# Kernel optimization log

Measured on AMD Instinct MI355X. Metric: run time of the kernel, lower is better.

The kernel has to match this reference:

```python
import jax, jax.numpy as jnp
import numpy as np

B, T, N = 2, 512, 512
H = 64          # hidden_dim
S = 8           # static_dim
C = 8           # coord_dim
DYN = 4         # dynamic feature dim (hard-coded in module)
SELF_LOOP_W = 1.0


def setup_inputs() -> dict:
    key = jax.random.key(0)
    ks = jax.random.split(key, 12)
    x = jax.random.normal(ks[0], (B, T, N), dtype=jnp.float32)
    mask = jax.random.randint(ks[1], (B, T, N), 0, 2).astype(jnp.float32)
    static_context = jax.random.normal(ks[2], (N, S), dtype=jnp.float32)
    node_coords = jax.random.normal(ks[3], (N, C), dtype=jnp.float32)
    sc = 0.1
    W1 = jax.random.normal(ks[4], (DYN + S, H), dtype=jnp.float32) * sc
    b1 = jnp.zeros((H,), dtype=jnp.float32)
    W2 = jax.random.normal(ks[5], (H, H), dtype=jnp.float32) * sc
    b2 = jnp.zeros((H,), dtype=jnp.float32)
    W3 = jax.random.normal(ks[6], (4 * H, H), dtype=jnp.float32) * sc
    b3 = jnp.zeros((H,), dtype=jnp.float32)
    W4 = jax.random.normal(ks[7], (H, 1), dtype=jnp.float32) * sc
    b4 = jnp.zeros((1,), dtype=jnp.float32)
    return {"x": x, "mask": mask, "static_context": static_context,
            "node_coords": node_coords, "W1": W1, "b1": b1, "W2": W2,
            "b2": b2, "W3": W3, "b3": b3, "W4": W4, "b4": b4}


def _dynamic_context(x, mask):
    observed = 1.0 - mask                                  # (B,T,N)
    count = jnp.maximum(observed.sum(axis=1), 1.0)          # (B,N)
    mean = (x * observed).sum(axis=1) / count               # (B,N)
    centered = (x - mean[:, None, :]) * observed
    std = jnp.sqrt((centered ** 2).sum(axis=1) / count + 1e-6)
    # last observed value per node
    t_idx = jnp.arange(x.shape[1], dtype=x.dtype)[None, :, None]
    latest = jnp.argmax(t_idx * observed, axis=1)           # (B,N) int
    last = jnp.take_along_axis(x, latest[:, None, :], axis=1)[:, 0, :]
    missing_ratio = mask.mean(axis=1)                       # (B,N)
    return jnp.stack([mean, std, last, missing_ratio], axis=-1)  # (B,N,4)


def _prior_adjacency(node_coords):
    diff = node_coords[:, None, :] - node_coords[None, :, :]  # (N,N,C)
    d2 = (diff ** 2).sum(-1)
    dist = jnp.where(d2 > 0, jnp.sqrt(jnp.where(d2 > 0, d2, 1.0)), 0.0)
    prior = 1.0 / (1.0 + dist)
    eye = jnp.eye(node_coords.shape[0], dtype=node_coords.dtype)
    return prior * (1.0 - eye)


def reference(x, mask, static_context, node_coords, W1, b1, W2, b2, W3, b3, W4, b4):
    batch = x.shape[0]
    node_dynamic = _dynamic_context(x, mask)                         # (B,N,4)
    node_static = jnp.broadcast_to(static_context[None], (batch,) + static_context.shape)
    feats = jnp.concatenate([node_dynamic, node_static], axis=-1)    # (B,N,4+S)
    h = jax.nn.relu(feats @ W1 + b1)
    node_repr = jax.nn.relu(h @ W2 + b2)                              # (B,N,H)

    h_i = node_repr[:, :, None, :]                                    # (B,N,1,H)
    h_j = node_repr[:, None, :, :]                                    # (B,1,N,H)
    hi = jnp.broadcast_to(h_i, (batch, N, N, H))
    hj = jnp.broadcast_to(h_j, (batch, N, N, H))
    pair = jnp.concatenate([hi, hj, jnp.abs(hi - hj), hi * hj], axis=-1)  # (B,N,N,4H)
    e = jax.nn.relu(pair @ W3 + b3)
    edge_mod = jax.nn.relu((e @ W4 + b4)[..., 0])                     # (B,N,N)

    prior = _prior_adjacency(node_coords)[None]                       # (1,N,N)
    eye = jnp.eye(N, dtype=x.dtype)[None]
    adapt = edge_mod * prior + eye * SELF_LOOP_W
    degree = jnp.maximum(adapt.sum(axis=-1), 1e-6)                    # (B,N)
    inv_sqrt = degree ** -0.5
    return inv_sqrt[:, :, None] * adapt * inv_sqrt[:, None, :]
```

## Files before the change

### kernel.cpp

```cpp
#include <hip/hip_runtime.h>
#include <hip/hip_bf16.h>
#include <math.h>

#define B_ 2
#define T_ 512
#define N_ 512
#define H_ 64

typedef __attribute__((ext_vector_type(8))) short short8;
typedef __attribute__((ext_vector_type(4))) float floatx4;

__device__ inline short f2bf(float f) {
    union { float f; unsigned u; } v; v.f = f;
    unsigned r = (v.u + 0x7fffu + ((v.u >> 16) & 1u)) >> 16;
    return (short)r;
}

__global__ void prep_kernel(const float* __restrict__ x, const float* __restrict__ mask,
                            const float* __restrict__ coords, const float* __restrict__ W3,
                            float* __restrict__ part, float* __restrict__ prior,
                            short* __restrict__ W3p) {
    int blk = blockIdx.x;
    if (blk < 512) {
        int b  = blk >> 8;
        int nc = (blk >> 5) & 7;
        int tc = blk & 31;
        int tn = threadIdx.x & 63;
        int tt = threadIdx.x >> 6;
        int n  = nc * 64 + tn;

        float sx = 0.f, sxx = 0.f, cnt = 0.f, msum = 0.f, bv = 0.f, bt = -1.f;
#pragma unroll
        for (int it = 0; it < 4; it++) {
            int t = tc * 16 + it * 4 + tt;
            int off = (b * T_ + t) * N_ + n;
            float xv = x[off];
            float mv = mask[off];
            float obs = 1.f - mv;
            sx   += xv * obs;
            sxx  += xv * xv * obs;
            cnt  += obs;
            msum += mv;
            if (obs > 0.5f) { bt = (float)t; bv = xv; }
        }

        __shared__ float red[6][4][64];
        red[0][tt][tn] = sx;  red[1][tt][tn] = sxx; red[2][tt][tn] = cnt;
        red[3][tt][tn] = msum; red[4][tt][tn] = bv; red[5][tt][tn] = bt;
        __syncthreads();

        if (threadIdx.x < 64) {
            float Sx = 0.f, Sxx = 0.f, Cnt = 0.f, Ms = 0.f, Bv = 0.f, Bt = -1.f;
#pragma unroll
            for (int u = 0; u < 4; u++) {
                Sx  += red[0][u][tn];
                Sxx += red[1][u][tn];
                Cnt += red[2][u][tn];
                Ms  += red[3][u][tn];
                float btu = red[5][u][tn];
                if (btu > Bt) { Bt = btu; Bv = red[4][u][tn]; }
            }
            const int plane = B_ * 32 * N_;
            int base = (b * 32 + tc) * N_ + n;
            part[0 * plane + base] = Sx;
            part[1 * plane + base] = Sxx;
            part[2 * plane + base] = Cnt;
            part[3 * plane + base] = Ms;
            part[4 * plane + base] = Bv;
            part[5 * plane + base] = Bt;
        }
    } else if (blk < 1536) {
        int idx = (blk - 512) * 256 + threadIdx.x;
        int i = idx >> 9, j = idx & (N_ - 1);
        float d2 = 0.f;
#pragma unroll
        for (int c = 0; c < 8; c++) {
            float df = coords[i * 8 + c] - coords[j * 8 + c];
            d2 += df * df;
        }
        float dist = (d2 > 0.f) ? sqrtf(d2) : 0.f;
        prior[idx] = (i == j) ? 0.f : 1.f / (1.f + dist);
    } else {
        int k = (blk - 1536) * 256 + threadIdx.x;
        int t = k & 7;
        int l = (k >> 3) & 63;
        int f = k >> 9;
        int s = f >> 2, nt = f & 3;
        int quad = l >> 4, col = l & 15;
        W3p[k] = f2bf(W3[(128 + s * 32 + quad * 8 + t) * H_ + nt * 16 + col]);
    }
}

__global__ __launch_bounds__(64) void node_kernel(
        const float* __restrict__ part, const float* __restrict__ x,
        const float* __restrict__ sc,
        const float* __restrict__ W1, const float* __restrict__ b1,
        const float* __restrict__ W2, const float* __restrict__ b2,
        const float* __restrict__ W3,
        float* __restrict__ nr, float* __restrict__ P, float* __restrict__ Qp) {
    int blk = blockIdx.x;
    int b = blk >> 9;
    int n = blk & (N_ - 1);
    int o = threadIdx.x;

    __shared__ float f[12];
    __shared__ float h[H_];
    __shared__ float r[H_];

    {
        const int plane = B_ * 32 * N_;
        float Sx = 0.f, Sxx = 0.f, Cnt = 0.f, Ms = 0.f, Bv = 0.f, Bt = -1.f;
        if (o < 32) {
            int base = (b * 32 + o) * N_ + n;
            Sx  = part[0 * plane + base];
            Sxx = part[1 * plane + base];
            Cnt = part[2 * plane + base];
            Ms  = part[3 * plane + base];
            Bv  = part[4 * plane + base];
            Bt  = part[5 * plane + base];
        }
#pragma unroll
        for (int off = 1; off < 32; off <<= 1) {
            Sx  += __shfl_xor(Sx, off);
            Sxx += __shfl_xor(Sxx, off);
            Cnt += __shfl_xor(Cnt, off);
            Ms  += __shfl_xor(Ms, off);
            float obt = __shfl_xor(Bt, off);
            float obv = __shfl_xor(Bv, off);
            if (obt > Bt) { Bt = obt; Bv = obv; }
        }
        if (o == 0) {
            float count = fmaxf(Cnt, 1.f);
            float mean  = Sx / count;
            float var   = (Sxx - 2.f * mean * Sx + mean * mean * Cnt) / count;
            float stdv  = sqrtf(fmaxf(var, 0.f) + 1e-6f);
            float last  = (Bt >= 0.f) ? Bv : x[b * T_ * N_ + n];
            f[0] = mean; f[1] = stdv; f[2] = last; f[3] = Ms * (1.f / (float)T_);
        }
        if (o >= 4 && o < 12) f[o] = sc[n * 8 + (o - 4)];
    }
    __syncthreads();

    float a = b1[o];
#pragma unroll
    for (int k = 0; k < 12; k++) a += f[k] * W1[k * H_ + o];
    h[o] = fmaxf(a, 0.f);
    __syncthreads();

    float a2 = b2[o];
#pragma unroll 8
    for (int k = 0; k < H_; k++) a2 += h[k] * W2[k * H_ + o];
    float rv = fmaxf(a2, 0.f);
    r[o] = rv;
    nr[(b * N_ + n) * H_ + o] = rv;
    __syncthreads();

    float p = 0.f, q = 0.f;
#pragma unroll 8
    for (int k = 0; k < H_; k++) {
        float rk = r[k];
        p += rk * W3[k * H_ + o];
        q += rk * W3[(H_ + k) * H_ + o];
    }
    P[(b * N_ + n) * H_ + o] = p;
    Qp[(b * N_ + n) * H_ + (o & 15) * 4 + (o >> 4)] = q;
}

__global__ __launch_bounds__(256) void pair_mfma_kernel(
        const float* __restrict__ nr, const float* __restrict__ P,
        const float* __restrict__ Qp, const short* __restrict__ W3p,
        const float* __restrict__ b3, const float* __restrict__ W4,
        const float* __restrict__ b4, const float* __restrict__ prior,
        float* __restrict__ adapt, float* __restrict__ degree) {
    int blk = blockIdx.x;
    int b = blk >> 9;
    int i = blk & (N_ - 1);
    int tid = threadIdx.x;
    int w = tid >> 6;
    int l = tid & 63;
    int col = l & 15;
    int quad = l >> 4;

    short8 bf[4][4];
#pragma unroll
    for (int s = 0; s < 4; s++)
#pragma unroll
        for (int nt = 0; nt < 4; nt++)
            bf[s][nt] = *(const short8*)(W3p + (((s * 4 + nt) * 64 + l) << 3));

    const float* hi_row = nr + (b * N_ + i) * H_;
    floatx4 hiA0 = *(const floatx4*)(hi_row + quad * 8);
    floatx4 hiA1 = *(const floatx4*)(hi_row + quad * 8 + 4);
    floatx4 hiB0 = *(const floatx4*)(hi_row + 32 + quad * 8);
    floatx4 hiB1 = *(const floatx4*)(hi_row + 32 + quad * 8 + 4);

    float pb3[4], w4v[4];
#pragma unroll
    for (int nt = 0; nt < 4; nt++) {
        int o = nt * 16 + col;
        pb3[nt] = P[(b * N_ + i) * H_ + o] + b3[o];
        w4v[nt] = W4[o];
    }
    float b4s = b4[0];
    const float* prow = prior + i * N_;
    const float* nrb = nr + (b * N_) * H_;
    float rsum = 0.f;

    floatx4 hA0, hA1, hB0, hB1;
    {
        const float* p0 = nrb + (w * 128 + col) * H_;
        hA0 = *(const floatx4*)(p0 + quad * 8);
        hA1 = *(const floatx4*)(p0 + quad * 8 + 4);
        hB0 = *(const floatx4*)(p0 + 32 + quad * 8);
        hB1 = *(const floatx4*)(p0 + 32 + quad * 8 + 4);
    }

#pragma unroll
    for (int mt = 0; mt < 8; mt++) {
        int j0 = w * 128 + mt * 16;

        floatx4 nA0, nA1, nB0, nB1;
        if (mt < 7) {
            const float* pn = nrb + (j0 + 16 + col) * H_;
            nA0 = *(const floatx4*)(pn + quad * 8);
            nA1 = *(const floatx4*)(pn + quad * 8 + 4);
            nB0 = *(const floatx4*)(pn + 32 + quad * 8);
            nB1 = *(const floatx4*)(pn + 32 + quad * 8 + 4);
        }

        floatx4 pv = *(const floatx4*)(prow + j0 + quad * 4);
        floatx4 qv[4];
#pragma unroll
        for (int r = 0; r < 4; r++)
            qv[r] = *(const floatx4*)(Qp + (b * N_ + j0 + quad * 4 + r) * H_ + col * 4);

        union { short8 s; __hip_bfloat162 h[4]; } a0, a1, a2, a3;
#pragma unroll
        for (int t = 0; t < 2; t++) {
            a0.h[t]     = __float22bfloat162_rn(make_float2(fabsf(hiA0[2*t] - hA0[2*t]),
                                                            fabsf(hiA0[2*t+1] - hA0[2*t+1])));
            a0.h[t + 2] = __float22bfloat162_rn(make_float2(fabsf(hiA1[2*t] - hA1[2*t]),
                                                            fabsf(hiA1[2*t+1] - hA1[2*t+1])));
            a1.h[t]     = __float22bfloat162_rn(make_float2(fabsf(hiB0[2*t] - hB0[2*t]),
                                                            fabsf(hiB0[2*t+1] - hB0[2*t+1])));
            a1.h[t + 2] = __float22bfloat162_rn(make_float2(fabsf(hiB1[2*t] - hB1[2*t]),
                                                            fabsf(hiB1[2*t+1] - hB1[2*t+1])));
            a2.h[t]     = __float22bfloat162_rn(make_float2(hiA0[2*t] * hA0[2*t],
                                                            hiA0[2*t+1] * hA0[2*t+1]));
            a2.h[t + 2] = __float22bfloat162_rn(make_float2(hiA1[2*t] * hA1[2*t],
                                                            hiA1[2*t+1] * hA1[2*t+1]));
            a3.h[t]     = __float22bfloat162_rn(make_float2(hiB0[2*t] * hB0[2*t],
                                                            hiB0[2*t+1] * hB0[2*t+1]));
            a3.h[t + 2] = __float22bfloat162_rn(make_float2(hiB1[2*t] * hB1[2*t],
                                                            hiB1[2*t+1] * hB1[2*t+1]));
        }

        floatx4 acc[4];
#pragma unroll
        for (int nt = 0; nt < 4; nt++) acc[nt] = (floatx4){0.f, 0.f, 0.f, 0.f};
#pragma unroll
        for (int nt = 0; nt < 4; nt++) {
            acc[nt] = __builtin_amdgcn_mfma_f32_16x16x32_bf16(a0.s, bf[0][nt], acc[nt], 0, 0, 0);
            acc[nt] = __builtin_amdgcn_mfma_f32_16x16x32_bf16(a1.s, bf[1][nt], acc[nt], 0, 0, 0);
            acc[nt] = __builtin_amdgcn_mfma_f32_16x16x32_bf16(a2.s, bf[2][nt], acc[nt], 0, 0, 0);
            acc[nt] = __builtin_amdgcn_mfma_f32_16x16x32_bf16(a3.s, bf[3][nt], acc[nt], 0, 0, 0);
        }

        float ed[4];
#pragma unroll
        for (int r = 0; r < 4; r++) {
            int j = j0 + quad * 4 + r;
            float p = 0.f;
#pragma unroll
            for (int nt = 0; nt < 4; nt++)
                p += fmaxf(acc[nt][r] + pb3[nt] + qv[r][nt], 0.f) * w4v[nt];
            p += __shfl_xor(p, 1);
            p += __shfl_xor(p, 2);
            p += __shfl_xor(p, 4);
            p += __shfl_xor(p, 8);
            float edge = fmaxf(p + b4s, 0.f);
            float ad = (j == i) ? 1.0f : edge * pv[r];
            ed[r] = ad;
            rsum += ad;
        }
        if (col == 0) {
            *(floatx4*)&adapt[(size_t)(b * N_ + i) * N_ + j0 + quad * 4] =
                (floatx4){ed[0], ed[1], ed[2], ed[3]};
        }

        if (mt < 7) { hA0 = nA0; hA1 = nA1; hB0 = nB0; hB1 = nB1; }
    }

    rsum += __shfl_xor(rsum, 16);
    rsum += __shfl_xor(rsum, 32);
    __shared__ float sRow[4];
    if (l == 0) sRow[w] = rsum;
    __syncthreads();
    if (tid == 0) degree[b * N_ + i] = sRow[0] + sRow[1] + sRow[2] + sRow[3];
}

__global__ void norm_kernel(const float* __restrict__ adapt, const float* __restrict__ deg,
                            float* __restrict__ out) {
    int idx = blockIdx.x * 256 + threadIdx.x;
    int b = idx >> 16;
    int r = (idx >> 7) & (N_ - 1);
    int c4 = (idx & 127) << 2;
    float dr = rsqrtf(fmaxf(deg[b * N_ + r], 1e-6f));
    floatx4 a = *(const floatx4*)(adapt + ((size_t)idx << 2));
    floatx4 o;
#pragma unroll
    for (int k = 0; k < 4; k++)
        o[k] = dr * a[k] * rsqrtf(fmaxf(deg[b * N_ + c4 + k], 1e-6f));
    *(floatx4*)(out + ((size_t)idx << 2)) = o;
}

extern "C" void kernel_launch(void* const* d_in, const int* in_sizes, int n_in,
                              void* d_out, int out_size, void* d_ws, size_t ws_size,
                              hipStream_t stream) {
    const float* x      = (const float*)d_in[0];
    const float* mask   = (const float*)d_in[1];
    const float* sc     = (const float*)d_in[2];
    const float* coords = (const float*)d_in[3];
    const float* W1 = (const float*)d_in[4];
    const float* b1 = (const float*)d_in[5];
    const float* W2 = (const float*)d_in[6];
    const float* b2 = (const float*)d_in[7];
    const float* W3 = (const float*)d_in[8];
    const float* b3 = (const float*)d_in[9];
    const float* W4 = (const float*)d_in[10];
    const float* b4 = (const float*)d_in[11];
    float* out = (float*)d_out;

    float* wsp = (float*)d_ws;
    float* nr    = wsp;
    float* P     = wsp + 65536;
    float* Qp    = wsp + 131072;
    float* prior = wsp + 196608;
    short* W3p   = (short*)(wsp + 458752);
    float* deg   = wsp + 462848;
    float* adapt = wsp + 463872;
    float* part  = adapt;

    prep_kernel<<<1568, 256, 0, stream>>>(x, mask, coords, W3, part, prior, W3p);
    node_kernel<<<B_ * N_, 64, 0, stream>>>(part, x, sc, W1, b1, W2, b2, W3, nr, P, Qp);
    pair_mfma_kernel<<<B_ * N_, 256, 0, stream>>>(nr, P, Qp, W3p, b3, W4, b4, prior, adapt, deg);
    norm_kernel<<<512, 256, 0, stream>>>(adapt, deg, out);
}
```

Measured before the change: 119.2 us.

## Fuse four kernels into one persistent kernel with grid-wide atomic barriers

```diff
diff --git a/kernel.cpp b/kernel.cpp
--- a/kernel.cpp
+++ b/kernel.cpp
@@ -6,6 +6,7 @@
 #define T_ 512
 #define N_ 512
 #define H_ 64
+#define NBLK 512u
 
 typedef __attribute__((ext_vector_type(8))) short short8;
 typedef __attribute__((ext_vector_type(4))) float floatx4;
@@ -16,17 +17,42 @@
     return (short)r;
 }
 
-__global__ void prep_kernel(const float* __restrict__ x, const float* __restrict__ mask,
-                            const float* __restrict__ coords, const float* __restrict__ W3,
-                            float* __restrict__ part, float* __restrict__ prior,
-                            short* __restrict__ W3p) {
+__device__ inline void gbar(unsigned* cnt, unsigned target) {
+    __syncthreads();
+    if (threadIdx.x == 0) {
+        __threadfence();
+        atomicAdd(cnt, 1u);
+        while (__hip_atomic_load(cnt, __ATOMIC_RELAXED, __HIP_MEMORY_SCOPE_AGENT) < target)
+            __builtin_amdgcn_s_sleep(1);
+        __threadfence();
+    }
+    __syncthreads();
+}
+
+__global__ __launch_bounds__(256, 2) void fused_kernel(
+        const float* __restrict__ x, const float* __restrict__ mask,
+        const float* __restrict__ sc, const float* __restrict__ coords,
+        const float* __restrict__ W1, const float* __restrict__ b1,
+        const float* __restrict__ W2, const float* __restrict__ b2,
+        const float* __restrict__ W3, const float* __restrict__ b3,
+        const float* __restrict__ W4, const float* __restrict__ b4,
+        float* __restrict__ part, float* __restrict__ prior,
+        short* __restrict__ W3p, float* __restrict__ nr,
+        float* __restrict__ P, float* __restrict__ Qp,
+        float* __restrict__ adapt, float* __restrict__ deg,
+        float* __restrict__ out, unsigned* __restrict__ bar) {
     int blk = blockIdx.x;
-    if (blk < 512) {
+    int tid = threadIdx.x;
+
+    __shared__ float red[6][4][64];
+    __shared__ float sRow[2][4];
+
+    {
         int b  = blk >> 8;
         int nc = (blk >> 5) & 7;
         int tc = blk & 31;
-        int tn = threadIdx.x & 63;
-        int tt = threadIdx.x >> 6;
+        int tn = tid & 63;
+        int tt = tid >> 6;
         int n  = nc * 64 + tn;
 
         float sx = 0.f, sxx = 0.f, cnt = 0.f, msum = 0.f, bv = 0.f, bt = -1.f;
@@ -43,13 +69,10 @@
             msum += mv;
             if (obs > 0.5f) { bt = (float)t; bv = xv; }
         }
-
-        __shared__ float red[6][4][64];
         red[0][tt][tn] = sx;  red[1][tt][tn] = sxx; red[2][tt][tn] = cnt;
         red[3][tt][tn] = msum; red[4][tt][tn] = bv; red[5][tt][tn] = bt;
         __syncthreads();
-
-        if (threadIdx.x < 64) {
+        if (tid < 64) {
             float Sx = 0.f, Sxx = 0.f, Cnt = 0.f, Ms = 0.f, Bv = 0.f, Bt = -1.f;
 #pragma unroll
             for (int u = 0; u < 4; u++) {
@@ -69,249 +92,238 @@
             part[4 * plane + base] = Bv;
             part[5 * plane + base] = Bt;
         }
-    } else if (blk < 1536) {
-        int idx = (blk - 512) * 256 + threadIdx.x;
-        int i = idx >> 9, j = idx & (N_ - 1);
-        float d2 = 0.f;
-#pragma unroll
-        for (int c = 0; c < 8; c++) {
-            float df = coords[i * 8 + c] - coords[j * 8 + c];
-            d2 += df * df;
-        }
-        float dist = (d2 > 0.f) ? sqrtf(d2) : 0.f;
-        prior[idx] = (i == j) ? 0.f : 1.f / (1.f + dist);
-    } else {
-        int k = (blk - 1536) * 256 + threadIdx.x;
-        int t = k & 7;
-        int l = (k >> 3) & 63;
-        int f = k >> 9;
-        int s = f >> 2, nt = f & 3;
-        int quad = l >> 4, col = l & 15;
-        W3p[k] = f2bf(W3[(128 + s * 32 + quad * 8 + t) * H_ + nt * 16 + col]);
-    }
-}
-
-__global__ __launch_bounds__(64) void node_kernel(
-        const float* __restrict__ part, const float* __restrict__ x,
-        const float* __restrict__ sc,
-        const float* __restrict__ W1, const float* __restrict__ b1,
-        const float* __restrict__ W2, const float* __restrict__ b2,
-        const float* __restrict__ W3,
-        float* __restrict__ nr, float* __restrict__ P, float* __restrict__ Qp) {
-    int blk = blockIdx.x;
-    int b = blk >> 9;
-    int n = blk & (N_ - 1);
-    int o = threadIdx.x;
-
-    __shared__ float f[12];
-    __shared__ float h[H_];
-    __shared__ float r[H_];
+
+#pragma unroll
+        for (int v = 0; v < 2; v++) {
+            int idx = blk * 512 + v * 256 + tid;
+            int pi = idx >> 9, pj = idx & (N_ - 1);
+            float d2 = 0.f;
+#pragma unroll
+            for (int c = 0; c < 8; c++) {
+                float df = coords[pi * 8 + c] - coords[pj * 8 + c];
+                d2 += df * df;
+            }
+            float dist = (d2 > 0.f) ? sqrtf(d2) : 0.f;
+            prior[idx] = (pi == pj) ? 0.f : 1.f / (1.f + dist);
+        }
+
+        if (tid < 16) {
+            int k = blk * 16 + tid;
+            int t = k & 7;
+            int l = (k >> 3) & 63;
+            int f = k >> 9;
+            int s = f >> 2, nt = f & 3;
+            int quad = l >> 4, col = l & 15;
+            W3p[k] = f2bf(W3[(128 + s * 32 + quad * 8 + t) * H_ + nt * 16 + col]);
+        }
+    }
+    gbar(bar + 0, NBLK);
 
     {
-        const int plane = B_ * 32 * N_;
-        float Sx = 0.f, Sxx = 0.f, Cnt = 0.f, Ms = 0.f, Bv = 0.f, Bt = -1.f;
-        if (o < 32) {
-            int base = (b * 32 + o) * N_ + n;
-            Sx  = part[0 * plane + base];
-            Sxx = part[1 * plane + base];
-            Cnt = part[2 * plane + base];
-            Ms  = part[3 * plane + base];
-            Bv  = part[4 * plane + base];
-            Bt  = part[5 * plane + base];
-        }
-#pragma unroll
-        for (int off = 1; off < 32; off <<= 1) {
-            Sx  += __shfl_xor(Sx, off);
-            Sxx += __shfl_xor(Sxx, off);
-            Cnt += __shfl_xor(Cnt, off);
-            Ms  += __shfl_xor(Ms, off);
-            float obt = __shfl_xor(Bt, off);
-            float obv = __shfl_xor(Bv, off);
-            if (obt > Bt) { Bt = obt; Bv = obv; }
-        }
-        if (o == 0) {
+        int wv = tid >> 6;
+        int o  = tid & 63;
+        if ((wv & 1) == 0) {
+            int b = wv >> 1;
+            int n = blk;
+            const int plane = B_ * 32 * N_;
+            int base = (b * 32 + (o & 31)) * N_ + n;
+            float Sx  = part[0 * plane + base];
+            float Sxx = part[1 * plane + base];
+            float Cnt = part[2 * plane + base];
+            float Ms  = part[3 * plane + base];
+            float Bv  = part[4 * plane + base];
+            float Bt  = part[5 * plane + base];
+#pragma unroll
+            for (int off = 1; off < 32; off <<= 1) {
+                Sx  += __shfl_xor(Sx, off);
+                Sxx += __shfl_xor(Sxx, off);
+                Cnt += __shfl_xor(Cnt, off);
+                Ms  += __shfl_xor(Ms, off);
+                float obt = __shfl_xor(Bt, off);
+                float obv = __shfl_xor(Bv, off);
+                if (obt > Bt) { Bt = obt; Bv = obv; }
+            }
             float count = fmaxf(Cnt, 1.f);
             float mean  = Sx / count;
             float var   = (Sxx - 2.f * mean * Sx + mean * mean * Cnt) / count;
             float stdv  = sqrtf(fmaxf(var, 0.f) + 1e-6f);
             float last  = (Bt >= 0.f) ? Bv : x[b * T_ * N_ + n];
-            f[0] = mean; f[1] = stdv; f[2] = last; f[3] = Ms * (1.f / (float)T_);
-        }
-        if (o >= 4 && o < 12) f[o] = sc[n * 8 + (o - 4)];
-    }
-    __syncthreads();
-
-    float a = b1[o];
-#pragma unroll
-    for (int k = 0; k < 12; k++) a += f[k] * W1[k * H_ + o];
-    h[o] = fmaxf(a, 0.f);
-    __syncthreads();
-
-    float a2 = b2[o];
-#pragma unroll 8
-    for (int k = 0; k < H_; k++) a2 += h[k] * W2[k * H_ + o];
-    float rv = fmaxf(a2, 0.f);
-    r[o] = rv;
-    nr[(b * N_ + n) * H_ + o] = rv;
-    __syncthreads();
-
-    float p = 0.f, q = 0.f;
-#pragma unroll 8
-    for (int k = 0; k < H_; k++) {
-        float rk = r[k];
-        p += rk * W3[k * H_ + o];
-        q += rk * W3[(H_ + k) * H_ + o];
-    }
-    P[(b * N_ + n) * H_ + o] = p;
-    Qp[(b * N_ + n) * H_ + (o & 15) * 4 + (o >> 4)] = q;
-}
-
-__global__ __launch_bounds__(256) void pair_mfma_kernel(
-        const float* __restrict__ nr, const float* __restrict__ P,
-        const float* __restrict__ Qp, const short* __restrict__ W3p,
-        const float* __restrict__ b3, const float* __restrict__ W4,
-        const float* __restrict__ b4, const float* __restrict__ prior,
-        float* __restrict__ adapt, float* __restrict__ degree) {
-    int blk = blockIdx.x;
-    int b = blk >> 9;
-    int i = blk & (N_ - 1);
-    int tid = threadIdx.x;
-    int w = tid >> 6;
-    int l = tid & 63;
-    int col = l & 15;
-    int quad = l >> 4;
-
-    short8 bf[4][4];
-#pragma unroll
-    for (int s = 0; s < 4; s++)
-#pragma unroll
-        for (int nt = 0; nt < 4; nt++)
-            bf[s][nt] = *(const short8*)(W3p + (((s * 4 + nt) * 64 + l) << 3));
-
-    const float* hi_row = nr + (b * N_ + i) * H_;
-    floatx4 hiA0 = *(const floatx4*)(hi_row + quad * 8);
-    floatx4 hiA1 = *(const floatx4*)(hi_row + quad * 8 + 4);
-    floatx4 hiB0 = *(const floatx4*)(hi_row + 32 + quad * 8);
-    floatx4 hiB1 = *(const floatx4*)(hi_row + 32 + quad * 8 + 4);
-
-    float pb3[4], w4v[4];
-#pragma unroll
-    for (int nt = 0; nt < 4; nt++) {
-        int o = nt * 16 + col;
-        pb3[nt] = P[(b * N_ + i) * H_ + o] + b3[o];
-        w4v[nt] = W4[o];
-    }
-    float b4s = b4[0];
-    const float* prow = prior + i * N_;
-    const float* nrb = nr + (b * N_) * H_;
-    float rsum = 0.f;
-
-    floatx4 hA0, hA1, hB0, hB1;
+            float mr    = Ms * (1.f / (float)T_);
+
+            float a = b1[o] + mean * W1[o] + stdv * W1[H_ + o] +
+                      last * W1[2 * H_ + o] + mr * W1[3 * H_ + o];
+#pragma unroll
+            for (int c = 0; c < 8; c++)
+                a += sc[n * 8 + c] * W1[(4 + c) * H_ + o];
+            float h = fmaxf(a, 0.f);
+
+            float a2 = b2[o];
+#pragma unroll 16
+            for (int k = 0; k < H_; k++)
+                a2 += __shfl(h, k) * W2[k * H_ + o];
+            float rv = fmaxf(a2, 0.f);
+            nr[(b * N_ + n) * H_ + o] = rv;
+
+            float p = 0.f, q = 0.f;
+#pragma unroll 16
+            for (int k = 0; k < H_; k++) {
+                float rk = __shfl(rv, k);
+                p += rk * W3[k * H_ + o];
+                q += rk * W3[(H_ + k) * H_ + o];
+            }
+            P[(b * N_ + n) * H_ + o] = p;
+            Qp[(b * N_ + n) * H_ + (o & 15) * 4 + (o >> 4)] = q;
+        }
+    }
+    gbar(bar + 1, NBLK);
+
     {
-        const float* p0 = nrb + (w * 128 + col) * H_;
-        hA0 = *(const floatx4*)(p0 + quad * 8);
-        hA1 = *(const floatx4*)(p0 + quad * 8 + 4);
-        hB0 = *(const floatx4*)(p0 + 32 + quad * 8);
-        hB1 = *(const floatx4*)(p0 + 32 + quad * 8 + 4);
-    }
-
-#pragma unroll
-    for (int mt = 0; mt < 8; mt++) {
-        int j0 = w * 128 + mt * 16;
-
-        floatx4 nA0, nA1, nB0, nB1;
-        if (mt < 7) {
-            const float* pn = nrb + (j0 + 16 + col) * H_;
-            nA0 = *(const floatx4*)(pn + quad * 8);
-            nA1 = *(const floatx4*)(pn + quad * 8 + 4);
-            nB0 = *(const floatx4*)(pn + 32 + quad * 8);
-            nB1 = *(const floatx4*)(pn + 32 + quad * 8 + 4);
-        }
-
-        floatx4 pv = *(const floatx4*)(prow + j0 + quad * 4);
-        floatx4 qv[4];
-#pragma unroll
-        for (int r = 0; r < 4; r++)
-            qv[r] = *(const floatx4*)(Qp + (b * N_ + j0 + quad * 4 + r) * H_ + col * 4);
-
-        union { short8 s; __hip_bfloat162 h[4]; } a0, a1, a2, a3;
-#pragma unroll
-        for (int t = 0; t < 2; t++) {
-            a0.h[t]     = __float22bfloat162_rn(make_float2(fabsf(hiA0[2*t] - hA0[2*t]),
-                                                            fabsf(hiA0[2*t+1] - hA0[2*t+1])));
-            a0.h[t + 2] = __float22bfloat162_rn(make_float2(fabsf(hiA1[2*t] - hA1[2*t]),
-                                                            fabsf(hiA1[2*t+1] - hA1[2*t+1])));
-            a1.h[t]     = __float22bfloat162_rn(make_float2(fabsf(hiB0[2*t] - hB0[2*t]),
-                                                            fabsf(hiB0[2*t+1] - hB0[2*t+1])));
-            a1.h[t + 2] = __float22bfloat162_rn(make_float2(fabsf(hiB1[2*t] - hB1[2*t]),
-                                                            fabsf(hiB1[2*t+1] - hB1[2*t+1])));
-            a2.h[t]     = __float22bfloat162_rn(make_float2(hiA0[2*t] * hA0[2*t],
-                                                            hiA0[2*t+1] * hA0[2*t+1]));
-            a2.h[t + 2] = __float22bfloat162_rn(make_float2(hiA1[2*t] * hA1[2*t],
-                                                            hiA1[2*t+1] * hA1[2*t+1]));
-            a3.h[t]     = __float22bfloat162_rn(make_float2(hiB0[2*t] * hB0[2*t],
-                                                            hiB0[2*t+1] * hB0[2*t+1]));
-            a3.h[t + 2] = __float22bfloat162_rn(make_float2(hiB1[2*t] * hB1[2*t],
-                                                            hiB1[2*t+1] * hB1[2*t+1]));
-        }
-
-        floatx4 acc[4];
-#pragma unroll
-        for (int nt = 0; nt < 4; nt++) acc[nt] = (floatx4){0.f, 0.f, 0.f, 0.f};
-#pragma unroll
-        for (int nt = 0; nt < 4; nt++) {
-            acc[nt] = __builtin_amdgcn_mfma_f32_16x16x32_bf16(a0.s, bf[0][nt], acc[nt], 0, 0, 0);
-            acc[nt] = __builtin_amdgcn_mfma_f32_16x16x32_bf16(a1.s, bf[1][nt], acc[nt], 0, 0, 0);
-            acc[nt] = __builtin_amdgcn_mfma_f32_16x16x32_bf16(a2.s, bf[2][nt], acc[nt], 0, 0, 0);
-            acc[nt] = __builtin_amdgcn_mfma_f32_16x16x32_bf16(a3.s, bf[3][nt], acc[nt], 0, 0, 0);
-        }
-
-        float ed[4];
-#pragma unroll
-        for (int r = 0; r < 4; r++) {
-            int j = j0 + quad * 4 + r;
-            float p = 0.f;
+        int i = blk;
+        int w = tid >> 6;
+        int l = tid & 63;
+        int col = l & 15;
+        int quad = l >> 4;
+
+        short8 bf[4][4];
+#pragma unroll
+        for (int s = 0; s < 4; s++)
 #pragma unroll
             for (int nt = 0; nt < 4; nt++)
-                p += fmaxf(acc[nt][r] + pb3[nt] + qv[r][nt], 0.f) * w4v[nt];
-            p += __shfl_xor(p, 1);
-            p += __shfl_xor(p, 2);
-            p += __shfl_xor(p, 4);
-            p += __shfl_xor(p, 8);
-            float edge = fmaxf(p + b4s, 0.f);
-            float ad = (j == i) ? 1.0f : edge * pv[r];
-            ed[r] = ad;
-            rsum += ad;
-        }
-        if (col == 0) {
-            *(floatx4*)&adapt[(size_t)(b * N_ + i) * N_ + j0 + quad * 4] =
-                (floatx4){ed[0], ed[1], ed[2], ed[3]};
-        }
-
-        if (mt < 7) { hA0 = nA0; hA1 = nA1; hB0 = nB0; hB1 = nB1; }
-    }
-
-    rsum += __shfl_xor(rsum, 16);
-    rsum += __shfl_xor(rsum, 32);
-    __shared__ float sRow[4];
-    if (l == 0) sRow[w] = rsum;
-    __syncthreads();
-    if (tid == 0) degree[b * N_ + i] = sRow[0] + sRow[1] + sRow[2] + sRow[3];
-}
-
-__global__ void norm_kernel(const float* __restrict__ adapt, const float* __restrict__ deg,
-                            float* __restrict__ out) {
-    int idx = blockIdx.x * 256 + threadIdx.x;
-    int b = idx >> 16;
-    int r = (idx >> 7) & (N_ - 1);
-    int c4 = (idx & 127) << 2;
-    float dr = rsqrtf(fmaxf(deg[b * N_ + r], 1e-6f));
-    floatx4 a = *(const floatx4*)(adapt + ((size_t)idx << 2));
-    floatx4 o;
-#pragma unroll
-    for (int k = 0; k < 4; k++)
-        o[k] = dr * a[k] * rsqrtf(fmaxf(deg[b * N_ + c4 + k], 1e-6f));
-    *(floatx4*)(out + ((size_t)idx << 2)) = o;
+                bf[s][nt] = *(const short8*)(W3p + (((s * 4 + nt) * 64 + l) << 3));
+
+        float w4v[4];
+#pragma unroll
+        for (int nt = 0; nt < 4; nt++) w4v[nt] = W4[nt * 16 + col];
+        float b4s = b4[0];
+        const float* prow = prior + i * N_;
+
+        float rs[2];
+#pragma unroll
+        for (int rb = 0; rb < 2; rb++) {
+            const float* hi_row = nr + (rb * N_ + i) * H_;
+            floatx4 hiA0 = *(const floatx4*)(hi_row + quad * 8);
+            floatx4 hiA1 = *(const floatx4*)(hi_row + quad * 8 + 4);
+            floatx4 hiB0 = *(const floatx4*)(hi_row + 32 + quad * 8);
+            floatx4 hiB1 = *(const floatx4*)(hi_row + 32 + quad * 8 + 4);
+
+            float pb3[4];
+#pragma unroll
+            for (int nt = 0; nt < 4; nt++) {
+                int o = nt * 16 + col;
+                pb3[nt] = P[(rb * N_ + i) * H_ + o] + b3[o];
+            }
+            const float* nrb = nr + (rb * N_) * H_;
+            float rsum = 0.f;
+
+            floatx4 hA0, hA1, hB0, hB1;
+            {
+                const float* p0 = nrb + (w * 128 + col) * H_;
+                hA0 = *(const floatx4*)(p0 + quad * 8);
+                hA1 = *(const floatx4*)(p0 + quad * 8 + 4);
+                hB0 = *(const floatx4*)(p0 + 32 + quad * 8);
+                hB1 = *(const floatx4*)(p0 + 32 + quad * 8 + 4);
+            }
+
+#pragma unroll
+            for (int mt = 0; mt < 8; mt++) {
+                int j0 = w * 128 + mt * 16;
+
+                floatx4 nA0, nA1, nB0, nB1;
+                if (mt < 7) {
+                    const float* pn = nrb + (j0 + 16 + col) * H_;
+                    nA0 = *(const floatx4*)(pn + quad * 8);
+                    nA1 = *(const floatx4*)(pn + quad * 8 + 4);
+                    nB0 = *(const floatx4*)(pn + 32 + quad * 8);
+                    nB1 = *(const floatx4*)(pn + 32 + quad * 8 + 4);
+                }
+
+                floatx4 pv = *(const floatx4*)(prow + j0 + quad * 4);
+                floatx4 qv[4];
+#pragma unroll
+                for (int r = 0; r < 4; r++)
+                    qv[r] = *(const floatx4*)(Qp + (rb * N_ + j0 + quad * 4 + r) * H_ + col * 4);
+
+                union { short8 s; __hip_bfloat162 h[4]; } a0, a1, a2, a3;
+#pragma unroll
+                for (int t = 0; t < 2; t++) {
+                    a0.h[t]     = __float22bfloat162_rn(make_float2(fabsf(hiA0[2*t] - hA0[2*t]),
+                                                                    fabsf(hiA0[2*t+1] - hA0[2*t+1])));
+                    a0.h[t + 2] = __float22bfloat162_rn(make_float2(fabsf(hiA1[2*t] - hA1[2*t]),
+                                                                    fabsf(hiA1[2*t+1] - hA1[2*t+1])));
+                    a1.h[t]     = __float22bfloat162_rn(make_float2(fabsf(hiB0[2*t] - hB0[2*t]),
+                                                                    fabsf(hiB0[2*t+1] - hB0[2*t+1])));
+                    a1.h[t + 2] = __float22bfloat162_rn(make_float2(fabsf(hiB1[2*t] - hB1[2*t]),
+                                                                    fabsf(hiB1[2*t+1] - hB1[2*t+1])));
+                    a2.h[t]     = __float22bfloat162_rn(make_float2(hiA0[2*t] * hA0[2*t],
+                                                                    hiA0[2*t+1] * hA0[2*t+1]));
+                    a2.h[t + 2] = __float22bfloat162_rn(make_float2(hiA1[2*t] * hA1[2*t],
+                                                                    hiA1[2*t+1] * hA1[2*t+1]));
+                    a3.h[t]     = __float22bfloat162_rn(make_float2(hiB0[2*t] * hB0[2*t],
+                                                                    hiB0[2*t+1] * hB0[2*t+1]));
+                    a3.h[t + 2] = __float22bfloat162_rn(make_float2(hiB1[2*t] * hB1[2*t],
+                                                                    hiB1[2*t+1] * hB1[2*t+1]));
+                }
+
+                floatx4 acc[4];
+#pragma unroll
+                for (int nt = 0; nt < 4; nt++) acc[nt] = (floatx4){0.f, 0.f, 0.f, 0.f};
+#pragma unroll
+                for (int nt = 0; nt < 4; nt++) {
+                    acc[nt] = __builtin_amdgcn_mfma_f32_16x16x32_bf16(a0.s, bf[0][nt], acc[nt], 0, 0, 0);
+                    acc[nt] = __builtin_amdgcn_mfma_f32_16x16x32_bf16(a1.s, bf[1][nt], acc[nt], 0, 0, 0);
+                    acc[nt] = __builtin_amdgcn_mfma_f32_16x16x32_bf16(a2.s, bf[2][nt], acc[nt], 0, 0, 0);
+                    acc[nt] = __builtin_amdgcn_mfma_f32_16x16x32_bf16(a3.s, bf[3][nt], acc[nt], 0, 0, 0);
+                }
+
+                float ed[4];
+#pragma unroll
+                for (int r = 0; r < 4; r++) {
+                    int j = j0 + quad * 4 + r;
+                    float p = 0.f;
+#pragma unroll
+                    for (int nt = 0; nt < 4; nt++)
+                        p += fmaxf(acc[nt][r] + pb3[nt] + qv[r][nt], 0.f) * w4v[nt];
+                    p += __shfl_xor(p, 1);
+                    p += __shfl_xor(p, 2);
+                    p += __shfl_xor(p, 4);
+                    p += __shfl_xor(p, 8);
+                    float edge = fmaxf(p + b4s, 0.f);
+                    float ad = (j == i) ? 1.0f : edge * pv[r];
+                    ed[r] = ad;
+                    rsum += ad;
+                }
+                if (col == 0) {
+                    *(floatx4*)&adapt[(size_t)(rb * N_ + i) * N_ + j0 + quad * 4] =
+                        (floatx4){ed[0], ed[1], ed[2], ed[3]};
+                }
+                if (mt < 7) { hA0 = nA0; hA1 = nA1; hB0 = nB0; hB1 = nB1; }
+            }
+
+            rsum += __shfl_xor(rsum, 16);
+            rsum += __shfl_xor(rsum, 32);
+            rs[rb] = rsum;
+        }
+
+        if (l == 0) { sRow[0][w] = rs[0]; sRow[1][w] = rs[1]; }
+        __syncthreads();
+        if (tid < 2)
+            deg[tid * N_ + i] = sRow[tid][0] + sRow[tid][1] + sRow[tid][2] + sRow[tid][3];
+    }
+    gbar(bar + 2, NBLK);
+
+    {
+        int idx = blk * 256 + tid;
+        int b = idx >> 16;
+        int r = (idx >> 7) & (N_ - 1);
+        int c4 = (idx & 127) << 2;
+        float dr = rsqrtf(fmaxf(deg[b * N_ + r], 1e-6f));
+        floatx4 a = *(const floatx4*)(adapt + ((size_t)idx << 2));
+        floatx4 o;
+#pragma unroll
+        for (int k = 0; k < 4; k++)
+            o[k] = dr * a[k] * rsqrtf(fmaxf(deg[b * N_ + c4 + k], 1e-6f));
+        *(floatx4*)(out + ((size_t)idx << 2)) = o;
+    }
 }
 
 extern "C" void kernel_launch(void* const* d_in, const int* in_sizes, int n_in,
@@ -340,9 +352,11 @@
     float* deg   = wsp + 462848;
     float* adapt = wsp + 463872;
     float* part  = adapt;
-
-    prep_kernel<<<1568, 256, 0, stream>>>(x, mask, coords, W3, part, prior, W3p);
-    node_kernel<<<B_ * N_, 64, 0, stream>>>(part, x, sc, W1, b1, W2, b2, W3, nr, P, Qp);
-    pair_mfma_kernel<<<B_ * N_, 256, 0, stream>>>(nr, P, Qp, W3p, b3, W4, b4, prior, adapt, deg);
-    norm_kernel<<<512, 256, 0, stream>>>(adapt, deg, out);
+    unsigned* bar = (unsigned*)(wsp + 988160);
+
+    hipMemsetAsync((void*)bar, 0, 16, stream);
+
+    fused_kernel<<<NBLK, 256, 0, stream>>>(
+        x, mask, sc, coords, W1, b1, W2, b2, W3, b3, W4, b4,
+        part, prior, W3p, nr, P, Qp, adapt, deg, out, bar);
 }
```

After: 236.1 us. 1.98x slower.
